# Kernel optimization log

Hardware: AMD Instinct MI355X
Metric: run time of the kernel (lower is better)

## Reference

```python
import jax, jax.numpy as jnp
import numpy as np

K = 5                                   # kernel_sz
SIGMA_SPATIAL = 2.0
SIGMA_INTENSITY = 0.1
NEG_SS_DIV = -1.0 / (2.0 * SIGMA_SPATIAL ** 2.0)   # value stored in self.kernel (same for all K*K taps)
SI_DIV = 1.0 / (2.0 * SIGMA_INTENSITY ** 2.0)      # self.sigma_intensity_div


def setup_inputs() -> dict:
    key = jax.random.key(0)
    k1, k2 = jax.random.split(key)
    t = jax.random.uniform(k1, (2, 3, 720, 1280), dtype=jnp.float32)      # guide image in [0,1]
    vector_curr = jax.random.normal(k2, (2, 2, 720, 1280), dtype=jnp.float32)  # flow vectors
    return {"t": t, "vector_curr": vector_curr}


def _joint_bilateral(t, v):
    # Fused sliding-window formulation: instead of materializing (N,H,W,K^2,C)
    # unfold patches, loop over the K*K static offsets (zero padding = F.unfold default)
    # and accumulate the weighted sum / normalizer. Same math as the original.
    N, C, H, W = t.shape
    Cv = v.shape[1]
    p = K // 2
    tp = jnp.pad(t, ((0, 0), (0, 0), (p, p), (p, p)))
    vp = jnp.pad(v, ((0, 0), (0, 0), (p, p), (p, p)))
    num = jnp.zeros_like(v)                      # (N,Cv,H,W)
    den = jnp.zeros((N, 1, H, W), t.dtype)
    for dy in range(K):
        for dx in range(K):
            ts = jax.lax.slice(tp, (0, 0, dy, dx), (N, C, dy + H, dx + W))
            vs = jax.lax.slice(vp, (0, 0, dy, dx), (N, Cv, dy + H, dx + W))
            # intensity_diff summed over guide channels -> (N,1,H,W)
            intensity_diff = jnp.sum((t - ts) ** 2, axis=1, keepdims=True)
            # coeff = clamp(1 - |kernel - diff * sigma_intensity_div|, 0, 1)
            coeff = jnp.clip(1.0 - jnp.abs(NEG_SS_DIV - intensity_diff * SI_DIV), 0.0, 1.0)
            num = num + vs * coeff
            den = den + coeff
    return (num / den).astype(jnp.float16)       # original returns fp16 NCHW


def reference(t, vector_curr):
    return _joint_bilateral(t, vector_curr)
```

## Files before the change

### kernel.cpp

```cpp
#include <hip/hip_runtime.h>
#include <hip/hip_fp16.h>


constexpr int H_ = 720;
constexpr int W_ = 1280;
constexpr int HW = H_ * W_;
constexpr float COEF0 = 0.875f;
constexpr float SIDIV = 50.0f;

constexpr int TC = 136;
constexpr int TR = 12;
constexpr int NCHUNK = 5 * TR * (TC / 4);

__global__ __launch_bounds__(256)
void jbf_lds(const float* __restrict__ t, const float* __restrict__ v,
             float* __restrict__ out) {
    __shared__ float lds[5][TR][TC];

    const int bx = blockIdx.x % 10;
    const int by = (blockIdx.x / 10) % 90;
    const int n  = blockIdx.x / 900;
    const int gx0 = bx * 128;
    const int gy0 = by * 8;

    const float* tn = t + (size_t)n * 3 * HW;
    const float* vn = v + (size_t)n * 2 * HW;
    float*       on = out + (size_t)n * 2 * HW;

    const int tid = threadIdx.x;

#pragma unroll
    for (int it = 0; it < 8; ++it) {
        const int i = tid + it * 256;
        if (i < NCHUNK) {
            const int c4 = i % 34;
            const int rr = (i / 34) % TR;
            const int ch = i / (34 * TR);
            const int gy = gy0 - 2 + rr;
            const int gx = gx0 - 4 + 4 * c4;
            float4 val = make_float4(0.f, 0.f, 0.f, 0.f);
            if ((unsigned)gy < (unsigned)H_ && (unsigned)gx < (unsigned)(W_ - 3)) {
                const float* src = (ch < 3) ? (tn + (size_t)ch * HW)
                                            : (vn + (size_t)(ch - 3) * HW);
                val = *(const float4*)(src + gy * W_ + gx);
            }
            ((float4*)lds)[i] = val;
        }
    }
    __syncthreads();

    const int tx = tid & 31;
    const int ty = tid >> 5;
    const int lc = 4 * tx;

    float c0[4], c1[4], c2[4];
    *(float4*)c0 = *(const float4*)&lds[0][ty + 2][lc + 4];
    *(float4*)c1 = *(const float4*)&lds[1][ty + 2][lc + 4];
    *(float4*)c2 = *(const float4*)&lds[2][ty + 2][lc + 4];

    float num0[4] = {0.f, 0.f, 0.f, 0.f};
    float num1[4] = {0.f, 0.f, 0.f, 0.f};
    float den[4]  = {0.f, 0.f, 0.f, 0.f};

#pragma unroll 1
    for (int r = 0; r < 5; ++r) {
        const int lr = ty + r;
        float w0[12], w1[12], w2[12], u0[12], u1[12];
#pragma unroll
        for (int s = 0; s < 3; ++s) {
            *(float4*)(w0 + 4 * s) = *(const float4*)&lds[0][lr][lc + 4 * s];
            *(float4*)(w1 + 4 * s) = *(const float4*)&lds[1][lr][lc + 4 * s];
            *(float4*)(w2 + 4 * s) = *(const float4*)&lds[2][lr][lc + 4 * s];
            *(float4*)(u0 + 4 * s) = *(const float4*)&lds[3][lr][lc + 4 * s];
            *(float4*)(u1 + 4 * s) = *(const float4*)&lds[4][lr][lc + 4 * s];
        }
#pragma unroll
        for (int dx = 0; dx < 5; ++dx) {
#pragma unroll
            for (int j = 0; j < 4; ++j) {
                const int k = dx + j + 2;
                const float d0 = c0[j] - w0[k];
                const float d1 = c1[j] - w1[k];
                const float d2 = c2[j] - w2[k];
                float diff = d0 * d0;
                diff = fmaf(d1, d1, diff);
                diff = fmaf(d2, d2, diff);
                const float c = fmaxf(fmaf(diff, -SIDIV, COEF0), 0.f);
                num0[j] = fmaf(u0[k], c, num0[j]);
                num1[j] = fmaf(u1[k], c, num1[j]);
                den[j] += c;
            }
        }
    }

    float4 o0, o1;
    float* o0a = (float*)&o0;
    float* o1a = (float*)&o1;
#pragma unroll
    for (int j = 0; j < 4; ++j) {
        const float rcp = 1.f / den[j];
        o0a[j] = __half2float(__float2half(num0[j] * rcp));
        o1a[j] = __half2float(__float2half(num1[j] * rcp));
    }
    const int ctr = (gy0 + ty) * W_ + gx0 + 4 * tx;
    *(float4*)(on + ctr) = o0;
    *(float4*)(on + HW + ctr) = o1;
}

extern "C" void kernel_launch(void* const* d_in, const int* in_sizes, int n_in,
                              void* d_out, int out_size, void* d_ws, size_t ws_size,
                              hipStream_t stream) {
    const float* t = (const float*)d_in[0];
    const float* v = (const float*)d_in[1];
    float* out = (float*)d_out;

    jbf_lds<<<1800, 256, 0, stream>>>(t, v, out);
}
```

Baseline: 31.64 us.

## Compute two output rows per thread to reuse LDS window loads across rows

Each thread now computes two vertically adjacent output rows, and the tile grows to 16 output rows (20 halo rows). Each LDS window row is loaded once and used for both output rows, so LDS reads per output drop and the halo overhead of global loads shrinks. In exchange there are more live registers (two sets of accumulators and centers), a larger LDS footprint per block, and half as many blocks (900), which may lower occupancy and parallelism.

Measured after the change: 34.21 us. 8.1% more time.

```diff
diff --git a/kernel.cpp b/kernel.cpp
--- a/kernel.cpp
+++ b/kernel.cpp
@@ -9,19 +9,45 @@
 constexpr float SIDIV = 50.0f;
 
 constexpr int TC = 136;
-constexpr int TR = 12;
+constexpr int TR = 20;
 constexpr int NCHUNK = 5 * TR * (TC / 4);
 
-__global__ __launch_bounds__(256)
-void jbf_lds(const float* __restrict__ t, const float* __restrict__ v,
-             float* __restrict__ out) {
+#define LOADW(LR)                                                              \
+    float w0[12], w1[12], w2[12], u0[12], u1[12];                              \
+    _Pragma("unroll") for (int s_ = 0; s_ < 3; ++s_) {                         \
+        *(float4*)(w0 + 4 * s_) = *(const float4*)&lds[0][LR][lc + 4 * s_];    \
+        *(float4*)(w1 + 4 * s_) = *(const float4*)&lds[1][LR][lc + 4 * s_];    \
+        *(float4*)(w2 + 4 * s_) = *(const float4*)&lds[2][LR][lc + 4 * s_];    \
+        *(float4*)(u0 + 4 * s_) = *(const float4*)&lds[3][LR][lc + 4 * s_];    \
+        *(float4*)(u1 + 4 * s_) = *(const float4*)&lds[4][LR][lc + 4 * s_];    \
+    }
+
+#define COMPW(C0, C1, C2, N0, N1, DN)                                          \
+    _Pragma("unroll") for (int dx_ = 0; dx_ < 5; ++dx_)                        \
+        _Pragma("unroll") for (int j_ = 0; j_ < 4; ++j_) {                     \
+            const int k_ = dx_ + j_ + 2;                                       \
+            const float d0_ = C0[j_] - w0[k_];                                 \
+            const float d1_ = C1[j_] - w1[k_];                                 \
+            const float d2_ = C2[j_] - w2[k_];                                 \
+            float diff_ = d0_ * d0_;                                           \
+            diff_ = fmaf(d1_, d1_, diff_);                                     \
+            diff_ = fmaf(d2_, d2_, diff_);                                     \
+            const float c_ = fmaxf(fmaf(diff_, -SIDIV, COEF0), 0.f);           \
+            N0[j_] = fmaf(u0[k_], c_, N0[j_]);                                 \
+            N1[j_] = fmaf(u1[k_], c_, N1[j_]);                                 \
+            DN[j_] += c_;                                                      \
+        }
+
+__global__ __launch_bounds__(256, 2)
+void jbf_dual(const float* __restrict__ t, const float* __restrict__ v,
+              float* __restrict__ out) {
     __shared__ float lds[5][TR][TC];
 
     const int bx = blockIdx.x % 10;
-    const int by = (blockIdx.x / 10) % 90;
-    const int n  = blockIdx.x / 900;
+    const int by = (blockIdx.x / 10) % 45;
+    const int n  = blockIdx.x / 450;
     const int gx0 = bx * 128;
-    const int gy0 = by * 8;
+    const int gy0 = by * 16;
 
     const float* tn = t + (size_t)n * 3 * HW;
     const float* vn = v + (size_t)n * 2 * HW;
@@ -30,7 +56,7 @@
     const int tid = threadIdx.x;
 
 #pragma unroll
-    for (int it = 0; it < 8; ++it) {
+    for (int it = 0; it < 14; ++it) {
         const int i = tid + it * 256;
         if (i < NCHUNK) {
             const int c4 = i % 34;
@@ -52,59 +78,53 @@
     const int tx = tid & 31;
     const int ty = tid >> 5;
     const int lc = 4 * tx;
+    const int r0 = 2 * ty;
 
-    float c0[4], c1[4], c2[4];
-    *(float4*)c0 = *(const float4*)&lds[0][ty + 2][lc + 4];
-    *(float4*)c1 = *(const float4*)&lds[1][ty + 2][lc + 4];
-    *(float4*)c2 = *(const float4*)&lds[2][ty + 2][lc + 4];
+    float cA0[4], cA1[4], cA2[4], cB0[4], cB1[4], cB2[4];
+    *(float4*)cA0 = *(const float4*)&lds[0][r0 + 2][lc + 4];
+    *(float4*)cA1 = *(const float4*)&lds[1][r0 + 2][lc + 4];
+    *(float4*)cA2 = *(const float4*)&lds[2][r0 + 2][lc + 4];
+    *(float4*)cB0 = *(const float4*)&lds[0][r0 + 3][lc + 4];
+    *(float4*)cB1 = *(const float4*)&lds[1][r0 + 3][lc + 4];
+    *(float4*)cB2 = *(const float4*)&lds[2][r0 + 3][lc + 4];
 
-    float num0[4] = {0.f, 0.f, 0.f, 0.f};
-    float num1[4] = {0.f, 0.f, 0.f, 0.f};
-    float den[4]  = {0.f, 0.f, 0.f, 0.f};
+    float nA0[4] = {0, 0, 0, 0}, nA1[4] = {0, 0, 0, 0}, dA[4] = {0, 0, 0, 0};
+    float nB0[4] = {0, 0, 0, 0}, nB1[4] = {0, 0, 0, 0}, dB[4] = {0, 0, 0, 0};
 
+    {
+        LOADW(r0)
+        COMPW(cA0, cA1, cA2, nA0, nA1, dA)
+    }
 #pragma unroll 1
-    for (int r = 0; r < 5; ++r) {
-        const int lr = ty + r;
-        float w0[12], w1[12], w2[12], u0[12], u1[12];
-#pragma unroll
-        for (int s = 0; s < 3; ++s) {
-            *(float4*)(w0 + 4 * s) = *(const float4*)&lds[0][lr][lc + 4 * s];
-            *(float4*)(w1 + 4 * s) = *(const float4*)&lds[1][lr][lc + 4 * s];
-            *(float4*)(w2 + 4 * s) = *(const float4*)&lds[2][lr][lc + 4 * s];
-            *(float4*)(u0 + 4 * s) = *(const float4*)&lds[3][lr][lc + 4 * s];
-            *(float4*)(u1 + 4 * s) = *(const float4*)&lds[4][lr][lc + 4 * s];
-        }
-#pragma unroll
-        for (int dx = 0; dx < 5; ++dx) {
-#pragma unroll
-            for (int j = 0; j < 4; ++j) {
-                const int k = dx + j + 2;
-                const float d0 = c0[j] - w0[k];
-                const float d1 = c1[j] - w1[k];
-                const float d2 = c2[j] - w2[k];
-                float diff = d0 * d0;
-                diff = fmaf(d1, d1, diff);
-                diff = fmaf(d2, d2, diff);
-                const float c = fmaxf(fmaf(diff, -SIDIV, COEF0), 0.f);
-                num0[j] = fmaf(u0[k], c, num0[j]);
-                num1[j] = fmaf(u1[k], c, num1[j]);
-                den[j] += c;
-            }
-        }
+    for (int s = 1; s <= 4; ++s) {
+        const int lr = r0 + s;
+        LOADW(lr)
+        COMPW(cA0, cA1, cA2, nA0, nA1, dA)
+        COMPW(cB0, cB1, cB2, nB0, nB1, dB)
+    }
+    {
+        LOADW(r0 + 5)
+        COMPW(cB0, cB1, cB2, nB0, nB1, dB)
     }
 
-    float4 o0, o1;
-    float* o0a = (float*)&o0;
-    float* o1a = (float*)&o1;
+    float4 oA0, oA1, oB0, oB1;
+    float* a0 = (float*)&oA0; float* a1 = (float*)&oA1;
+    float* b0 = (float*)&oB0; float* b1 = (float*)&oB1;
 #pragma unroll
     for (int j = 0; j < 4; ++j) {
-        const float rcp = 1.f / den[j];
-        o0a[j] = __half2float(__float2half(num0[j] * rcp));
-        o1a[j] = __half2float(__float2half(num1[j] * rcp));
+        const float ra = 1.f / dA[j];
+        const float rb = 1.f / dB[j];
+        a0[j] = __half2float(__float2half(nA0[j] * ra));
+        a1[j] = __half2float(__float2half(nA1[j] * ra));
+        b0[j] = __half2float(__float2half(nB0[j] * rb));
+        b1[j] = __half2float(__float2half(nB1[j] * rb));
     }
-    const int ctr = (gy0 + ty) * W_ + gx0 + 4 * tx;
-    *(float4*)(on + ctr) = o0;
-    *(float4*)(on + HW + ctr) = o1;
+    const int ctrA = (gy0 + r0) * W_ + gx0 + 4 * tx;
+    const int ctrB = ctrA + W_;
+    *(float4*)(on + ctrA) = oA0;
+    *(float4*)(on + HW + ctrA) = oA1;
+    *(float4*)(on + ctrB) = oB0;
+    *(float4*)(on + HW + ctrB) = oB1;
 }
 
 extern "C" void kernel_launch(void* const* d_in, const int* in_sizes, int n_in,
@@ -114,5 +134,5 @@
     const float* v = (const float*)d_in[1];
     float* out = (float*)d_out;
 
-    jbf_lds<<<1800, 256, 0, stream>>>(t, v, out);
+    jbf_dual<<<900, 256, 0, stream>>>(t, v, out);
 }
```
